# Kernel tuning notes

Measured on AMD Instinct MI355X. Metric: run time of the kernel, lower is better.

Reference implementation:

```python
import jax, jax.numpy as jnp
import numpy as np

B, S, D, H = 4, 2048, 1024, 16
DK = D // H


def setup_inputs() -> dict:
    key = jax.random.key(0)
    ks = jax.random.split(key, 12)
    def lin(k):
        # torch nn.Linear default init scale ~ 1/sqrt(fan_in); use small normal
        return jax.random.normal(k, (D, D), dtype=jnp.float32) * (1.0 / np.sqrt(D))
    inp = {
        "query": jax.random.normal(ks[0], (B, S, D), dtype=jnp.float32),
        "key":   jax.random.normal(ks[1], (B, S, D), dtype=jnp.float32),
        "value": jax.random.normal(ks[2], (B, S, D), dtype=jnp.float32),
        "Wq": lin(ks[3]), "bq": jax.random.normal(ks[4], (D,), dtype=jnp.float32) * 0.01,
        "Wk": lin(ks[5]), "bk": jax.random.normal(ks[6], (D,), dtype=jnp.float32) * 0.01,
        "Wv": lin(ks[7]), "bv": jax.random.normal(ks[8], (D,), dtype=jnp.float32) * 0.01,
        "Wo": lin(ks[9]), "bo": jax.random.normal(ks[10], (D,), dtype=jnp.float32) * 0.01,
        # causal mask, True = attend (masked_fill where mask == 0)
        "causal_mask": jnp.tril(jnp.ones((S, S), dtype=bool))[None, None, :, :],
    }
    return inp


def reference(query, key, value, Wq, bq, Wk, bk, Wv, bv, Wo, bo, causal_mask):
    # Linear projections (torch Linear: y = x @ W.T + b), split heads -> [B,H,S,DK]
    def proj(x, W, b):
        return (x @ W.T + b).reshape(B, S, H, DK).transpose(0, 2, 1, 3)
    Q = proj(query, Wq, bq)
    K = proj(key, Wk, bk)
    V = proj(value, Wv, bv)
    scale = 1.0 / jnp.sqrt(jnp.float32(DK))
    scores = jnp.einsum('bhqd,bhkd->bhqk', Q, K) * scale  # [B,H,S,S]
    scores = jnp.where(causal_mask, scores, -jnp.inf)
    attn = jax.nn.softmax(scores, axis=-1)
    out = jnp.einsum('bhqk,bhkd->bhqd', attn, V)  # [B,H,S,DK]
    out = out.transpose(0, 2, 1, 3).reshape(B, S, D)
    return out @ Wo.T + bo
```

## Files before the change

kernel.cpp:

```cpp
#include <hip/hip_runtime.h>
#include <stdint.h>

#define SLEN   2048
#define DMODEL 1024
#define NHEAD  16
#define DKH    64
#define BATCH  4

typedef unsigned short ushort_t;
typedef __bf16         bf16x8 __attribute__((ext_vector_type(8)));
typedef unsigned short u16x8  __attribute__((ext_vector_type(8)));
typedef unsigned short u16x4  __attribute__((ext_vector_type(4)));
typedef unsigned int   u32x4  __attribute__((ext_vector_type(4)));
typedef float          f32x4  __attribute__((ext_vector_type(4)));

#define QSCALE 0.18033688f

__device__ __forceinline__ ushort_t f2bf(float f) {
  unsigned int u = __builtin_bit_cast(unsigned int, f);
  u += 0x7fffu + ((u >> 16) & 1u);
  return (ushort_t)(u >> 16);
}
__device__ __forceinline__ unsigned pk2(float a, float b) {
  const unsigned ua = __builtin_bit_cast(unsigned, a) + 0x8000u;
  const unsigned ub = __builtin_bit_cast(unsigned, b) + 0x8000u;
  return __builtin_amdgcn_perm(ub, ua, 0x07060302u);
}
__device__ __forceinline__ u16x8 cvt8f(const float* p) {
  f32x4 a = *(const f32x4*)p;
  f32x4 b = *(const f32x4*)(p + 4);
  u32x4 w;
  w[0] = pk2(a[0], a[1]);
  w[1] = pk2(a[2], a[3]);
  w[2] = pk2(b[0], b[1]);
  w[3] = pk2(b[2], b[3]);
  return __builtin_bit_cast(u16x8, w);
}

typedef __attribute__((address_space(1))) void gvoid_t;
typedef __attribute__((address_space(3))) void lvoid_t;
__device__ __forceinline__ void gld_lds16(const void* g, void* l) {
  __builtin_amdgcn_global_load_lds((gvoid_t*)(g), (lvoid_t*)(l), 16, 0, 0);
}

__device__ __forceinline__ int swz(int row, int c) {
  return row * 64 + (c ^ ((row & 7) * 8));
}

__global__ __launch_bounds__(256) void cvt_all(
    const float* __restrict__ Wq, const float* __restrict__ Wk,
    const float* __restrict__ Wv, const float* __restrict__ Wo,
    const float* __restrict__ q, const float* __restrict__ k,
    const float* __restrict__ v,
    ushort_t* __restrict__ Wbf, ushort_t* __restrict__ Xq,
    ushort_t* __restrict__ Xk,  ushort_t* __restrict__ Xv) {
  const int b = blockIdx.x;
  if (b < 2048) {
    const int gid = b * 256 + threadIdx.x;
    const int seg = gid >> 17;
    const int off = (gid & 131071) * 8;
    const float* src = (seg == 0) ? Wq : (seg == 1) ? Wk : (seg == 2) ? Wv : Wo;
    *(u16x8*)&Wbf[((size_t)seg << 20) + off] = cvt8f(src + off);
  } else {
    const int gid = (b - 2048) * 256 + threadIdx.x;
    const int seg = gid >> 20;
    const size_t off = (size_t)(gid & 1048575) * 8;
    const float* src = (seg == 0) ? q : (seg == 1) ? k : v;
    ushort_t*    dst = (seg == 0) ? Xq : (seg == 1) ? Xk : Xv;
    *(u16x8*)&dst[off] = cvt8f(src + off);
  }
}

__device__ __forceinline__ void gemm_body(
    const ushort_t* __restrict__ X, const ushort_t* __restrict__ W,
    const float* __restrict__ bias, void* __restrict__ Outv, const int mode,
    const float sc)
{
  __shared__ ushort_t lA[2][128 * 32];
  __shared__ ushort_t lB[2][256 * 32];

  const int t    = threadIdx.x;
  const int lane = t & 63;
  const int w    = t >> 6;
  const int wm   = (w >> 1) * 64;
  const int wn   = (w & 1) * 128;
  const int m0   = blockIdx.x * 128;
  const int n0   = blockIdx.y * 256;
  const int col  = lane & 15;
  const int quad = lane >> 4;

  f32x4 acc[4][8];
#pragma unroll
  for (int i = 0; i < 4; i++)
#pragma unroll
    for (int j = 0; j < 8; j++) acc[i][j] = f32x4{0.f, 0.f, 0.f, 0.f};

  const int rA   = t >> 2;
  const int csrc = ((t & 3) ^ ((rA >> 1) & 3)) * 8;
  const ushort_t* gA0 = X + (size_t)(m0 + rA) * DMODEL + csrc;
  const ushort_t* gA1 = gA0 + (size_t)64 * DMODEL;
  const ushort_t* gB0 = W + (size_t)(n0 + rA) * DMODEL + csrc;
  const ushort_t* gB1 = gB0 + (size_t)64 * DMODEL;
  const ushort_t* gB2 = gB0 + (size_t)128 * DMODEL;
  const ushort_t* gB3 = gB0 + (size_t)192 * DMODEL;

#define STAGE_G(buf, k0) do {                        \
    gld_lds16(gB0 + (k0), &lB[buf][t * 8]);          \
    gld_lds16(gB1 + (k0), &lB[buf][t * 8 + 2048]);   \
    gld_lds16(gB2 + (k0), &lB[buf][t * 8 + 4096]);   \
    gld_lds16(gB3 + (k0), &lB[buf][t * 8 + 6144]);   \
    gld_lds16(gA0 + (k0), &lA[buf][t * 8]);          \
    gld_lds16(gA1 + (k0), &lA[buf][t * 8 + 2048]);   \
  } while (0)

  const int rchunk = (quad ^ ((col >> 1) & 3)) * 8;

  STAGE_G(0, 0);

  const int NT = DMODEL / 32;
  for (int ks = 0; ks < NT; ++ks) {
    const int cur = ks & 1;
    if (ks + 1 < NT) {
      STAGE_G(cur ^ 1, (ks + 1) * 32);
      asm volatile("s_waitcnt vmcnt(6)" ::: "memory");
    } else {
      asm volatile("s_waitcnt vmcnt(0)" ::: "memory");
    }
    __builtin_amdgcn_s_barrier();
    __builtin_amdgcn_sched_barrier(0);

    bf16x8 af[4], bfr[8];
#pragma unroll
    for (int mi = 0; mi < 4; mi++)
      af[mi] = __builtin_bit_cast(bf16x8,
          *(const u16x8*)&lA[cur][(wm + mi * 16 + col) * 32 + rchunk]);
#pragma unroll
    for (int ni = 0; ni < 8; ni++)
      bfr[ni] = __builtin_bit_cast(bf16x8,
          *(const u16x8*)&lB[cur][(wn + ni * 16 + col) * 32 + rchunk]);

#pragma unroll
    for (int mi = 0; mi < 4; mi++)
#pragma unroll
      for (int ni = 0; ni < 8; ni++)
        acc[mi][ni] = __builtin_amdgcn_mfma_f32_16x16x32_bf16(
            af[mi], bfr[ni], acc[mi][ni], 0, 0, 0);

    __builtin_amdgcn_s_barrier();
    __builtin_amdgcn_sched_barrier(0);
  }
#undef STAGE_G

  const int b_ = (m0 + wm) >> 11;

  if (mode == 1) {
    __syncthreads();
    ushort_t* tb = &lB[0][0] + w * 2176;
    float bns_[8];
#pragma unroll
    for (int ni = 0; ni < 8; ni++)
      bns_[ni] = bias[n0 + wn + ni * 16 + col] * sc;
    const int h0 = (n0 + wn) >> 6;
    const int sB = ((m0 + wm) & (SLEN - 1));
#pragma unroll
    for (int mi = 0; mi < 4; mi++) {
#pragma unroll
      for (int ni = 0; ni < 8; ni++)
#pragma unroll
        for (int r = 0; r < 4; r++)
          tb[(quad * 4 + r) * 136 + ni * 16 + col] =
              f2bf(fmaf(acc[mi][ni][r], sc, bns_[ni]));
      asm volatile("s_waitcnt lgkmcnt(0)" ::: "memory");
      __builtin_amdgcn_sched_barrier(0);
#pragma unroll
      for (int p = 0; p < 4; p++) {
        const int c   = p * 64 + lane;
        const int row = c >> 4;
        const int ch  = c & 15;
        u16x8 vv = *(const u16x8*)&tb[row * 136 + ch * 8];
        const int h  = h0 + (ch >> 3);
        const int dk = (ch & 7) * 8;
        const int s  = sB + mi * 16 + row;
        *(u16x8*)&((ushort_t*)Outv)[(((size_t)(b_ * NHEAD + h)) * SLEN + s) * DKH + dk] = vv;
      }
      asm volatile("s_waitcnt lgkmcnt(0)" ::: "memory");
      __builtin_amdgcn_sched_barrier(0);
    }
    return;
  }

#pragma unroll
  for (int ni = 0; ni < 8; ni++) {
    const int n  = n0 + wn + ni * 16 + col;
    const float bn = bias[n];
    const int h  = n >> 6, dk = n & (DKH - 1);
#pragma unroll
    for (int mi = 0; mi < 4; mi++) {
      if (mode == 2) {
        const int s0 = ((m0 + wm + mi * 16 + quad * 4) & (SLEN - 1));
        u16x4 pk;
#pragma unroll
        for (int r = 0; r < 4; r++) pk[r] = f2bf(acc[mi][ni][r] + bn);
        *(u16x4*)&((ushort_t*)Outv)[(((size_t)(b_ * NHEAD + h)) * DKH + dk) * SLEN + s0] = pk;
      } else {
#pragma unroll
        for (int r = 0; r < 4; r++) {
          const int m = m0 + wm + mi * 16 + quad * 4 + r;
          ((float*)Outv)[(size_t)m * DMODEL + n] = acc[mi][ni][r] + bn;
        }
      }
    }
  }
}

__global__ __launch_bounds__(256, 3) void gemm_qkv(
    const ushort_t* Xq, const ushort_t* Xk, const ushort_t* Xv,
    const ushort_t* Wbf,
    const float* bq, const float* bk, const float* bv,
    ushort_t* Qh, ushort_t* Kh, ushort_t* VhT) {
  const int z = blockIdx.z;
  const ushort_t* X = (z == 0) ? Xq : (z == 1) ? Xk : Xv;
  const ushort_t* W = Wbf + ((size_t)z << 20);
  const float* bias = (z == 0) ? bq : (z == 1) ? bk : bv;
  ushort_t* out     = (z == 0) ? Qh : (z == 1) ? Kh : VhT;
  gemm_body(X, W, bias, out, (z == 2) ? 2 : 1, (z == 0) ? QSCALE : 1.0f);
}

__global__ __launch_bounds__(256, 3) void gemm_out(
    const ushort_t* X, const ushort_t* Wobf, const float* bo, float* Out) {
  gemm_body(X, Wobf, bo, Out, 0, 1.0f);
}

__global__ __launch_bounds__(256, 4) void flash_attn(
    const ushort_t* __restrict__ Qh, const ushort_t* __restrict__ Kh,
    const ushort_t* __restrict__ VhT, ushort_t* __restrict__ Out)
{
  __shared__ ushort_t lK[2 * 64 * 64];
  __shared__ ushort_t lV[2 * 64 * 64];
  __shared__ ushort_t lP[4 * 16 * 64];

  const int t    = threadIdx.x;
  const int lane = t & 63;
  const int w    = t >> 6;
  const int col  = lane & 15;
  const int quad = lane >> 4;
  const int bh   = blockIdx.y;
  const int x    = blockIdx.x;
  const int ntA  = x + 1;
  const int ntB  = 32 - x;
  const int q0A  = x * 64;
  const int q0B  = (31 - x) * 64;

  const ushort_t* Qb = Qh  + (size_t)bh * SLEN * DKH;
  const ushort_t* Kb = Kh  + (size_t)bh * SLEN * DKH;
  const ushort_t* Vt = VhT + (size_t)bh * DKH * SLEN;

  bf16x8 qfA[2], qfB[2];
  {
    const int ra = q0A + w * 16 + col;
    const int rb = q0B + w * 16 + col;
    qfA[0] = __builtin_bit_cast(bf16x8, *(const u16x8*)&Qb[(size_t)ra * DKH + quad * 8]);
    qfA[1] = __builtin_bit_cast(bf16x8, *(const u16x8*)&Qb[(size_t)ra * DKH + 32 + quad * 8]);
    qfB[0] = __builtin_bit_cast(bf16x8, *(const u16x8*)&Qb[(size_t)rb * DKH + quad * 8]);
    qfB[1] = __builtin_bit_cast(bf16x8, *(const u16x8*)&Qb[(size_t)rb * DKH + 32 + quad * 8]);
  }

  f32x4 accA[4], accB[4], laccA, laccB;
#pragma unroll
  for (int n2 = 0; n2 < 4; n2++) {
    accA[n2] = f32x4{0.f, 0.f, 0.f, 0.f};
    accB[n2] = f32x4{0.f, 0.f, 0.f, 0.f};
  }
  laccA = f32x4{0.f, 0.f, 0.f, 0.f};
  laccB = f32x4{0.f, 0.f, 0.f, 0.f};

  u16x8 ones_u;
#pragma unroll
  for (int i = 0; i < 8; ++i) ones_u[i] = 0x3F80;
  const bf16x8 onesf = __builtin_bit_cast(bf16x8, ones_u);

  const int fA   = t * 8;
  const int rowA = fA >> 6;
  const int innA = fA & 63;
  const int cA   = innA ^ ((rowA & 7) * 8);
  const int rowB = rowA + 32;
  const int cB   = innA ^ ((rowB & 7) * 8);
  const ushort_t* gK0 = Kb + (size_t)rowA * DKH + cA;
  const ushort_t* gK1 = Kb + (size_t)rowB * DKH + cB;
  const ushort_t* gV0 = Vt + (size_t)rowA * SLEN + cA;
  const ushort_t* gV1 = Vt + (size_t)rowB * SLEN + cB;
  ushort_t* sK0 = &lK[fA];
  ushort_t* sK1 = &lK[fA + 2048];
  ushort_t* sV0 = &lV[fA];
  ushort_t* sV1 = &lV[fA + 2048];

  ushort_t* lPw = &lP[w * 1024];

  auto compute = [&](const bf16x8* qf, f32x4* acc_o, f32x4& lacc,
                     const int q0, const bool diag, const int kb,
                     const ushort_t* Kc, const ushort_t* Vc) {
    f32x4 sacc[4];
#pragma unroll
    for (int nt = 0; nt < 4; nt++) sacc[nt] = f32x4{0.f, 0.f, 0.f, 0.f};
#pragma unroll
    for (int ks = 0; ks < 2; ++ks) {
#pragma unroll
      for (int nt = 0; nt < 4; ++nt) {
        bf16x8 kf = __builtin_bit_cast(bf16x8,
            *(const u16x8*)&Kc[swz(nt * 16 + col, ks * 32 + quad * 8)]);
        sacc[nt] = __builtin_amdgcn_mfma_f32_16x16x32_bf16(qf[ks], kf, sacc[nt], 0, 0, 0);
      }
    }
#pragma unroll
    for (int r = 0; r < 4; r++) {
#pragma unroll
      for (int nt = 0; nt < 4; nt++) {
        float p = exp2f(sacc[nt][r]);
        if (diag) {
          const int kg = kb + nt * 16 + col;
          const int qg = q0 + w * 16 + quad * 4 + r;
          if (kg > qg) p = 0.f;
        }
        lPw[swz(quad * 4 + r, nt * 16 + col)] = f2bf(p);
      }
    }
    asm volatile("s_waitcnt lgkmcnt(0)" ::: "memory");
#pragma unroll
    for (int ks = 0; ks < 2; ++ks) {
      bf16x8 pf = __builtin_bit_cast(bf16x8,
          *(const u16x8*)&lPw[swz(col, ks * 32 + quad * 8)]);
      lacc = __builtin_amdgcn_mfma_f32_16x16x32_bf16(pf, onesf, lacc, 0, 0, 0);
#pragma unroll
      for (int n2 = 0; n2 < 4; ++n2) {
        bf16x8 vf = __builtin_bit_cast(bf16x8,
            *(const u16x8*)&Vc[swz(n2 * 16 + col, ks * 32 + quad * 8)]);
        acc_o[n2] = __builtin_amdgcn_mfma_f32_16x16x32_bf16(pf, vf, acc_o[n2], 0, 0, 0);
      }
    }
  };

  gld_lds16(gK0, sK0);
  gld_lds16(gK1, sK1);
  gld_lds16(gV0, sV0);
  gld_lds16(gV1, sV1);

  for (int it = 0; it < ntB; ++it) {
    const int cur = it & 1;
    const int kb  = it * 64;
    const ushort_t* Kc = &lK[cur * 4096];
    const ushort_t* Vc = &lV[cur * 4096];

    if (it + 1 < ntB) {
      const size_t kb1 = (size_t)(it + 1) * 64;
      const int nb = (cur ^ 1) * 4096;
      gld_lds16(gK0 + kb1 * DKH, sK0 + nb);
      gld_lds16(gK1 + kb1 * DKH, sK1 + nb);
      gld_lds16(gV0 + kb1,       sV0 + nb);
      gld_lds16(gV1 + kb1,       sV1 + nb);
      asm volatile("s_waitcnt vmcnt(4)" ::: "memory");
    } else {
      asm volatile("s_waitcnt vmcnt(0)" ::: "memory");
    }
    __builtin_amdgcn_s_barrier();

    compute(qfB, accB, laccB, q0B, it == ntB - 1, kb, Kc, Vc);
    if (it < ntA)
      compute(qfA, accA, laccA, q0A, it == ntA - 1, kb, Kc, Vc);

    __builtin_amdgcn_s_barrier();
  }

  const int b_ = bh >> 4;
  const int h  = bh & (NHEAD - 1);
#pragma unroll
  for (int side = 0; side < 2; ++side) {
    const f32x4* ao = side ? accA : accB;
    const f32x4& la = side ? laccA : laccB;
    const int q0 = side ? q0A : q0B;
#pragma unroll
    for (int r = 0; r < 4; r++) {
      const int qg = q0 + w * 16 + quad * 4 + r;
      const float inv = 1.f / la[r];
#pragma unroll
      for (int n2 = 0; n2 < 4; n2++) {
        const size_t oidx = ((size_t)b_ * SLEN + qg) * DMODEL + h * DKH + n2 * 16 + col;
        Out[oidx] = f2bf(ao[n2][r] * inv);
      }
    }
  }
}

extern "C" void kernel_launch(void* const* d_in, const int* in_sizes, int n_in,
                              void* d_out, int out_size, void* d_ws, size_t ws_size,
                              hipStream_t stream) {
  (void)in_sizes; (void)n_in; (void)out_size; (void)ws_size;
  const float* q  = (const float*)d_in[0];
  const float* k  = (const float*)d_in[1];
  const float* v  = (const float*)d_in[2];
  const float* Wq = (const float*)d_in[3];
  const float* bq = (const float*)d_in[4];
  const float* Wk = (const float*)d_in[5];
  const float* bk = (const float*)d_in[6];
  const float* Wv = (const float*)d_in[7];
  const float* bv = (const float*)d_in[8];
  const float* Wo = (const float*)d_in[9];
  const float* bo = (const float*)d_in[10];

  ushort_t* ws = (ushort_t*)d_ws;
  const size_t NELEM = (size_t)BATCH * SLEN * DMODEL;
  ushort_t* Wbf = ws;
  ushort_t* Qh  = ws + 4 * (1u << 20);
  ushort_t* Kh  = Qh + NELEM;
  ushort_t* Xq  = Kh + NELEM;
  ushort_t* Xk  = Xq + NELEM;
  ushort_t* Ao  = Xq;
  ushort_t* VhT = (ushort_t*)d_out;
  ushort_t* Xv  = (ushort_t*)d_out + NELEM;

  hipLaunchKernelGGL(cvt_all, dim3(2048 + 12288), dim3(256), 0, stream,
                     Wq, Wk, Wv, Wo, q, k, v, Wbf, Xq, Xk, Xv);
  hipLaunchKernelGGL(gemm_qkv, dim3(64, 4, 3), dim3(256), 0, stream,
                     Xq, Xk, Xv, Wbf, bq, bk, bv, Qh, Kh, VhT);
  hipLaunchKernelGGL(flash_attn, dim3(16, BATCH * NHEAD), dim3(256), 0, stream,
                     Qh, Kh, VhT, Ao);
  hipLaunchKernelGGL(gemm_out, dim3(64, 4), dim3(256), 0, stream,
                     Ao, Wbf + (3u << 20), bo, (float*)d_out);
}
```

Measured before the change: 384.3 us.

## Interleave both query tiles' MFMAs per key block and remap flash grid to XCDs

New measurement: 574.3 us. 1.49x slower.

```diff
diff --git a/kernel.cpp b/kernel.cpp
--- a/kernel.cpp
+++ b/kernel.cpp
@@ -244,8 +244,10 @@
   const int w    = t >> 6;
   const int col  = lane & 15;
   const int quad = lane >> 4;
-  const int bh   = blockIdx.y;
-  const int x    = blockIdx.x;
+  const int wg   = blockIdx.x;
+  const int flat = (wg & 7) * 128 + (wg >> 3);
+  const int bh   = flat >> 4;
+  const int x    = flat & 15;
   const int ntA  = x + 1;
   const int ntB  = 32 - x;
   const int q0A  = x * 64;
@@ -296,49 +298,6 @@
 
   ushort_t* lPw = &lP[w * 1024];
 
-  auto compute = [&](const bf16x8* qf, f32x4* acc_o, f32x4& lacc,
-                     const int q0, const bool diag, const int kb,
-                     const ushort_t* Kc, const ushort_t* Vc) {
-    f32x4 sacc[4];
-#pragma unroll
-    for (int nt = 0; nt < 4; nt++) sacc[nt] = f32x4{0.f, 0.f, 0.f, 0.f};
-#pragma unroll
-    for (int ks = 0; ks < 2; ++ks) {
-#pragma unroll
-      for (int nt = 0; nt < 4; ++nt) {
-        bf16x8 kf = __builtin_bit_cast(bf16x8,
-            *(const u16x8*)&Kc[swz(nt * 16 + col, ks * 32 + quad * 8)]);
-        sacc[nt] = __builtin_amdgcn_mfma_f32_16x16x32_bf16(qf[ks], kf, sacc[nt], 0, 0, 0);
-      }
-    }
-#pragma unroll
-    for (int r = 0; r < 4; r++) {
-#pragma unroll
-      for (int nt = 0; nt < 4; nt++) {
-        float p = exp2f(sacc[nt][r]);
-        if (diag) {
-          const int kg = kb + nt * 16 + col;
-          const int qg = q0 + w * 16 + quad * 4 + r;
-          if (kg > qg) p = 0.f;
-        }
-        lPw[swz(quad * 4 + r, nt * 16 + col)] = f2bf(p);
-      }
-    }
-    asm volatile("s_waitcnt lgkmcnt(0)" ::: "memory");
-#pragma unroll
-    for (int ks = 0; ks < 2; ++ks) {
-      bf16x8 pf = __builtin_bit_cast(bf16x8,
-          *(const u16x8*)&lPw[swz(col, ks * 32 + quad * 8)]);
-      lacc = __builtin_amdgcn_mfma_f32_16x16x32_bf16(pf, onesf, lacc, 0, 0, 0);
-#pragma unroll
-      for (int n2 = 0; n2 < 4; ++n2) {
-        bf16x8 vf = __builtin_bit_cast(bf16x8,
-            *(const u16x8*)&Vc[swz(n2 * 16 + col, ks * 32 + quad * 8)]);
-        acc_o[n2] = __builtin_amdgcn_mfma_f32_16x16x32_bf16(pf, vf, acc_o[n2], 0, 0, 0);
-      }
-    }
-  };
-
   gld_lds16(gK0, sK0);
   gld_lds16(gK1, sK1);
   gld_lds16(gV0, sV0);
@@ -363,9 +322,83 @@
     }
     __builtin_amdgcn_s_barrier();
 
-    compute(qfB, accB, laccB, q0B, it == ntB - 1, kb, Kc, Vc);
-    if (it < ntA)
-      compute(qfA, accA, laccA, q0A, it == ntA - 1, kb, Kc, Vc);
+    const bool doA = (it < ntA);
+    const bool dgB = (it == ntB - 1);
+    const bool dgA = (it == ntA - 1);
+
+    f32x4 sB[4], sA[4];
+#pragma unroll
+    for (int nt = 0; nt < 4; nt++) {
+      sB[nt] = f32x4{0.f, 0.f, 0.f, 0.f};
+      sA[nt] = f32x4{0.f, 0.f, 0.f, 0.f};
+    }
+    __builtin_amdgcn_s_setprio(1);
+#pragma unroll
+    for (int ks = 0; ks < 2; ++ks) {
+#pragma unroll
+      for (int nt = 0; nt < 4; ++nt) {
+        bf16x8 kf = __builtin_bit_cast(bf16x8,
+            *(const u16x8*)&Kc[swz(nt * 16 + col, ks * 32 + quad * 8)]);
+        sB[nt] = __builtin_amdgcn_mfma_f32_16x16x32_bf16(qfB[ks], kf, sB[nt], 0, 0, 0);
+        if (doA)
+          sA[nt] = __builtin_amdgcn_mfma_f32_16x16x32_bf16(qfA[ks], kf, sA[nt], 0, 0, 0);
+      }
+    }
+    __builtin_amdgcn_s_setprio(0);
+
+#pragma unroll
+    for (int r = 0; r < 4; r++) {
+#pragma unroll
+      for (int nt = 0; nt < 4; nt++) {
+        float p = exp2f(sB[nt][r]);
+        if (dgB) {
+          const int kg = kb + nt * 16 + col;
+          const int qg = q0B + w * 16 + quad * 4 + r;
+          if (kg > qg) p = 0.f;
+        }
+        lPw[swz(quad * 4 + r, nt * 16 + col)] = f2bf(p);
+      }
+    }
+    asm volatile("s_waitcnt lgkmcnt(0)" ::: "memory");
+    bf16x8 pfB[2], pfA[2];
+    pfB[0] = __builtin_bit_cast(bf16x8, *(const u16x8*)&lPw[swz(col, quad * 8)]);
+    pfB[1] = __builtin_bit_cast(bf16x8, *(const u16x8*)&lPw[swz(col, 32 + quad * 8)]);
+    asm volatile("s_waitcnt lgkmcnt(0)" ::: "memory");
+    if (doA) {
+#pragma unroll
+      for (int r = 0; r < 4; r++) {
+#pragma unroll
+        for (int nt = 0; nt < 4; nt++) {
+          float p = exp2f(sA[nt][r]);
+          if (dgA) {
+            const int kg = kb + nt * 16 + col;
+            const int qg = q0A + w * 16 + quad * 4 + r;
+            if (kg > qg) p = 0.f;
+          }
+          lPw[swz(quad * 4 + r, nt * 16 + col)] = f2bf(p);
+        }
+      }
+      asm volatile("s_waitcnt lgkmcnt(0)" ::: "memory");
+      pfA[0] = __builtin_bit_cast(bf16x8, *(const u16x8*)&lPw[swz(col, quad * 8)]);
+      pfA[1] = __builtin_bit_cast(bf16x8, *(const u16x8*)&lPw[swz(col, 32 + quad * 8)]);
+    }
+
+    __builtin_amdgcn_s_setprio(1);
+#pragma unroll
+    for (int ks = 0; ks < 2; ++ks) {
+      laccB = __builtin_amdgcn_mfma_f32_16x16x32_bf16(pfB[ks], onesf, laccB, 0, 0, 0);
+      if (doA)
+        laccA = __builtin_amdgcn_mfma_f32_16x16x32_bf16(pfA[ks], onesf, laccA, 0, 0, 0);
+#pragma unroll
+      for (int n2 = 0; n2 < 4; ++n2) {
+        bf16x8 vf = __builtin_bit_cast(bf16x8,
+            *(const u16x8*)&Vc[swz(n2 * 16 + col, ks * 32 + quad * 8)]);
+        accB[n2] = __builtin_amdgcn_mfma_f32_16x16x32_bf16(pfB[ks], vf, accB[n2], 0, 0, 0);
+        if (doA)
+          accA[n2] = __builtin_amdgcn_mfma_f32_16x16x32_bf16(pfA[ks], vf, accA[n2], 0, 0, 0);
+      }
+    }
+    __builtin_amdgcn_s_setprio(0);
 
     __builtin_amdgcn_s_barrier();
   }
@@ -421,7 +454,7 @@
                      Wq, Wk, Wv, Wo, q, k, v, Wbf, Xq, Xk, Xv);
   hipLaunchKernelGGL(gemm_qkv, dim3(64, 4, 3), dim3(256), 0, stream,
                      Xq, Xk, Xv, Wbf, bq, bk, bv, Qh, Kh, VhT);
-  hipLaunchKernelGGL(flash_attn, dim3(16, BATCH * NHEAD), dim3(256), 0, stream,
+  hipLaunchKernelGGL(flash_attn, dim3(1024), dim3(256), 0, stream,
                      Qh, Kh, VhT, Ao);
   hipLaunchKernelGGL(gemm_out, dim3(64, 4), dim3(256), 0, stream,
                      Ao, Wbf + (3u << 20), bo, (float*)d_out);
```
